# Kernel tuning notes

Hardware: AMD Instinct MI355X
Metric: run time of the kernel (lower is better)

The kernel has to match this reference:

```python
import jax, jax.numpy as jnp
import numpy as np

# head layout: lcmap(2) | lcoff(2) | lleng(1) | angle(1) -> head_off = [2,4,5,6]
NLINES = 1000       # top-K line centers per image (F-Clip default)
RESOLUTION = 128    # heatmap resolution (512 image / 4), M.resolution
S_NMS = 2.0         # structural NMS threshold, M.s_nms


def _heatmap_nms(h):
    # keep only 3x3 local maxima (standard center-point heatmap NMS)
    hmax = jax.lax.reduce_window(h, -jnp.inf, jax.lax.max, (3, 3), (1, 1), 'SAME')
    return jnp.where(h == hmax, h, 0.0)


def _fclip_single(lcmap, lcoff, lleng, angle):
    # lcmap (H,W); lcoff (2,H,W); lleng (H,W); angle (H,W)
    H, W = lcmap.shape
    score, idx = jax.lax.top_k(_heatmap_nms(lcmap).reshape(-1), NLINES)
    yi, xi = idx // W, idx % W
    # sub-pixel line center: integer cell + learned offset + 0.5
    yc = yi.astype(lcmap.dtype) + lcoff[0, yi, xi] + 0.5
    xc = xi.astype(lcmap.dtype) + lcoff[1, yi, xi] + 0.5
    half_len = lleng[yi, xi] * (RESOLUTION / 2.0)   # length normalized by res/2
    theta = angle[yi, xi] * jnp.pi                  # angle normalized [0,1] -> [0,pi]
    dy = half_len * jnp.sin(theta)
    dx = half_len * jnp.cos(theta)
    p1 = jnp.stack([yc - dy, xc - dx], axis=-1)     # (K,2) in (y,x)
    p2 = jnp.stack([yc + dy, xc + dx], axis=-1)
    lines = jnp.stack([p1, p2], axis=1)             # (K,2,2)
    return lines, score


def _structure_nms(lines, score, thr):
    # structural distance between lines = min over the two endpoint matchings
    p1, p2 = lines[:, 0], lines[:, 1]               # (K,2) each

    def sq(a, b):                                   # pairwise squared dists (K,K)
        return ((a[:, None, :] - b[None, :, :]) ** 2).sum(-1)

    dist = jnp.minimum(sq(p1, p1) + sq(p2, p2), sq(p1, p2) + sq(p2, p1))
    K = score.shape[0]
    i = jnp.arange(K)
    # scores arrive sorted descending from top_k: line j is suppressed by any
    # higher-scoring line i<j within the structural threshold
    suppress = jnp.any((dist <= thr) & (i[:, None] < i[None, :]), axis=0)
    return lines, jnp.where(suppress, 0.0, score)


def setup_inputs() -> dict:
    key = jax.random.key(0)
    # raw head logits from the backbone stack: (B, 6, H, W)
    output = jax.random.normal(key, (32, 6, 128, 128), dtype=jnp.float32)
    return {"output": output}


def reference(output):
    # GLSD.test_forward decode path
    lcmap = jax.nn.softmax(output[:, 0:2], axis=1)[:, 1]   # (B,H,W) center prob
    lcoff = jax.nn.sigmoid(output[:, 2:4]) - 0.5           # (B,2,H,W) offsets
    lleng = jax.nn.sigmoid(output[:, 4])                   # (B,H,W) half length
    angle = jax.nn.sigmoid(output[:, 5])                   # (B,H,W) angle
    lines, score = jax.vmap(_fclip_single)(lcmap, lcoff, lleng, angle)
    lines, score = jax.vmap(lambda l, s: _structure_nms(l, s, S_NMS))(lines, score)
    return lcmap, lcoff, lleng, angle, lines, score
```

## Files before the change

kernel.cpp:

```cpp
#include <hip/hip_runtime.h>
#include <math.h>

#define BATCH 32
#define HW 16384
#define WIDTH 128
#define NLINES 1000
#define NCAND 4096
#define CHUNK 1024
#define NCHUNK 4
#define SLOTS_PER_BLOCK 64

#define OFF_LCMAP 0
#define OFF_LCOFF (BATCH * HW)
#define OFF_LLENG (OFF_LCOFF + 2 * BATCH * HW)
#define OFF_ANGLE (OFF_LLENG + BATCH * HW)
#define OFF_LINES (OFF_ANGLE + BATCH * HW)
#define OFF_SCORE (OFF_LINES + BATCH * NLINES * 4)

#define WS_NEEDED ((size_t)BATCH * NCAND * 8)

#define PI_F 3.14159265358979323846f

#define NMS_KTILE 16
#define NMS_NSPLIT 16
#define NMS_SPLIT 63

__device__ __forceinline__ float sigmoidf_(float x) {
    return 1.0f / (1.0f + expf(-x));
}

__device__ __forceinline__ float softmax1(float x0, float x1) {
    float m = fmaxf(x0, x1);
    float e0 = expf(x0 - m);
    float e1 = expf(x1 - m);
    return e1 / (e0 + e1);
}

__device__ __forceinline__ unsigned long long pack_key(float v, unsigned p) {
    return ((unsigned long long)__float_as_uint(v) << 32)
         | (unsigned long long)(0xFFFFFFFFu - p);
}

__global__ __launch_bounds__(256) void prep_collect_kernel(
        const float* __restrict__ in, float* __restrict__ out,
        unsigned long long* __restrict__ wskeys) {
    __shared__ float sm[4][WIDTH];
    __shared__ int wcnt_s[4];
    __shared__ int wpre_s[4];
    __shared__ int tot_s;

    const int blk = blockIdx.x;
    const int b = blk >> 6;
    const int rp = blk & 63;
    const int y0 = rp * 2;
    const int r = threadIdx.x >> 7;
    const int c = threadIdx.x & (WIDTH - 1);
    const int y = y0 + r;
    const int p = y * WIDTH + c;
    const float* __restrict__ ib = in + (size_t)b * 6 * HW;

    float x0 = ib[p];
    float x1 = ib[HW + p];
    float x2 = ib[2 * HW + p];
    float x3 = ib[3 * HW + p];
    float x4 = ib[4 * HW + p];
    float x5 = ib[5 * HW + p];

    float v = softmax1(x0, x1);
    sm[1 + r][c] = v;
    {
        int hy = (r == 0) ? (y0 - 1) : (y0 + 2);
        int hyc = min(max(hy, 0), WIDTH - 1);
        int hp = hyc * WIDTH + c;
        sm[r == 0 ? 0 : 3][c] = softmax1(ib[hp], ib[HW + hp]);
    }

    out[OFF_LCMAP + b * HW + p] = v;
    out[OFF_LCOFF + b * 2 * HW + p]      = sigmoidf_(x2) - 0.5f;
    out[OFF_LCOFF + b * 2 * HW + HW + p] = sigmoidf_(x3) - 0.5f;
    out[OFF_LLENG + b * HW + p] = sigmoidf_(x4);
    out[OFF_ANGLE + b * HW + p] = sigmoidf_(x5);
    __syncthreads();

    const int ly = 1 + r;
    float m = -INFINITY;
    #pragma unroll
    for (int dy = -1; dy <= 1; ++dy) {
        #pragma unroll
        for (int dx = -1; dx <= 1; ++dx) {
            if (dy == 0 && dx == 0) continue;
            int yy = y + dy, xx = c + dx;
            int xc = min(max(xx, 0), WIDTH - 1);
            float nv = sm[ly + dy][xc];
            bool inb = ((unsigned)yy < (unsigned)WIDTH) & ((unsigned)xx < (unsigned)WIDTH);
            m = fmaxf(m, inb ? nv : -INFINITY);
        }
    }
    bool keep = (v >= m);

    unsigned long long mask = __ballot(keep);
    int lane = threadIdx.x & 63;
    int w = threadIdx.x >> 6;
    if (lane == 0) wcnt_s[w] = __popcll(mask);
    __syncthreads();
    if (threadIdx.x == 0) {
        int a0 = wcnt_s[0], a1 = wcnt_s[1], a2 = wcnt_s[2], a3 = wcnt_s[3];
        wpre_s[0] = 0; wpre_s[1] = a0; wpre_s[2] = a0 + a1; wpre_s[3] = a0 + a1 + a2;
        tot_s = a0 + a1 + a2 + a3;
    }
    __syncthreads();

    unsigned long long* __restrict__ gk =
        wskeys + (size_t)b * NCAND + (size_t)rp * SLOTS_PER_BLOCK;
    if (keep) {
        int pos = wpre_s[w] + __popcll(mask & ((1ULL << lane) - 1ULL));
        if (pos < SLOTS_PER_BLOCK)
            gk[pos] = pack_key(v, (unsigned)p);
    }
    int tot = tot_s < SLOTS_PER_BLOCK ? tot_s : SLOTS_PER_BLOCK;
    if (threadIdx.x < SLOTS_PER_BLOCK && threadIdx.x >= tot)
        gk[threadIdx.x] = 0ULL;
}

__global__ __launch_bounds__(512) void sort_chunks_kernel(
        unsigned long long* __restrict__ wskeys) {
    __shared__ unsigned long long sk[CHUNK];
    const int c = blockIdx.x, b = blockIdx.y;
    const int base = c * CHUNK;
    unsigned long long* gk = wskeys + (size_t)b * NCAND;

    for (int i = threadIdx.x; i < CHUNK; i += 512) sk[i] = gk[base + i];
    __syncthreads();

    for (int size = 2; size <= CHUNK; size <<= 1) {
        for (int stride = size >> 1; stride > 0; stride >>= 1) {
            int t = threadIdx.x;
            int i = ((t & ~(stride - 1)) << 1) | (t & (stride - 1));
            int j = i | stride;
            bool asc = (i & size) != 0;
            unsigned long long a = sk[i], cc = sk[j];
            if ((a < cc) != asc) { sk[i] = cc; sk[j] = a; }
            __syncthreads();
        }
    }
    for (int i = threadIdx.x; i < CHUNK; i += 512) gk[base + i] = sk[i];
}

__device__ bool keep_at(const float* __restrict__ L, int p) {
    int y = p >> 7, x = p & (WIDTH - 1);
    float v = L[p];
    for (int dy = -1; dy <= 1; ++dy) {
        int yy = y + dy;
        if (yy < 0 || yy >= WIDTH) continue;
        for (int dx = -1; dx <= 1; ++dx) {
            if (dy == 0 && dx == 0) continue;
            int xx = x + dx;
            if (xx < 0 || xx >= WIDTH) continue;
            if (L[yy * WIDTH + xx] > v) return false;
        }
    }
    return true;
}

__global__ __launch_bounds__(256) void merge_lines_kernel(
        float* __restrict__ out, const unsigned long long* __restrict__ wskeys) {
    __shared__ unsigned long long sk[NCAND];
    __shared__ int wsum[4];
    __shared__ int cnt_s;
    const int c = blockIdx.x, b = blockIdx.y;
    const unsigned long long* gk = wskeys + (size_t)b * NCAND;
    for (int i = threadIdx.x; i < NCAND; i += 256) sk[i] = gk[i];
    __syncthreads();

    const float* off0 = out + OFF_LCOFF + b * 2 * HW;
    const float* off1 = off0 + HW;
    const float* leng = out + OFF_LLENG + b * HW;
    const float* ang  = out + OFF_ANGLE + b * HW;

    #pragma unroll
    for (int q = 0; q < CHUNK / 256; ++q) {
        int lslot = q * 256 + threadIdx.x;
        int mslot = c * CHUNK + lslot;
        unsigned long long e = sk[mslot];
        if (e == 0ULL) continue;
        int rank = lslot;
        #pragma unroll
        for (int c2 = 0; c2 < NCHUNK; ++c2) {
            if (c2 == c) continue;
            const unsigned long long* A = sk + c2 * CHUNK;
            int lo = 0, hi = CHUNK;
            while (lo < hi) {
                int mid = (lo + hi) >> 1;
                if (A[mid] > e) lo = mid + 1; else hi = mid;
            }
            rank += lo;
        }
        if (rank < NLINES) {
            unsigned p = 0xFFFFFFFFu - (unsigned)(e & 0xFFFFFFFFull);
            float score = __uint_as_float((unsigned)(e >> 32));
            int yi = (int)(p >> 7), xi = (int)(p & (WIDTH - 1));
            float yc = (float)yi + off0[p] + 0.5f;
            float xc = (float)xi + off1[p] + 0.5f;
            float hl = leng[p] * 64.0f;
            float th = ang[p] * PI_F;
            float dy = hl * sinf(th);
            float dx = hl * cosf(th);
            float4 ln = make_float4(yc - dy, xc - dx, yc + dy, xc + dx);
            *(float4*)(out + OFF_LINES + (size_t)(b * NLINES + rank) * 4) = ln;
            out[OFF_SCORE + b * NLINES + rank] = score;
        }
    }

    if (c != 0) return;
    int local = 0;
    for (int i = threadIdx.x; i < NCAND; i += 256) local += (sk[i] != 0ULL);
    for (int off = 32; off; off >>= 1) local += __shfl_down(local, off);
    if ((threadIdx.x & 63) == 0) wsum[threadIdx.x >> 6] = local;
    __syncthreads();
    if (threadIdx.x == 0) cnt_s = wsum[0] + wsum[1] + wsum[2] + wsum[3];
    __syncthreads();
    const int cnt = cnt_s;
    if (cnt < NLINES && threadIdx.x == 0) {
        const float* L = out + OFF_LCMAP + b * HW;
        int rank = cnt;
        for (int p = 0; p < HW && rank < NLINES; ++p) {
            if (keep_at(L, p)) continue;
            int yi = p >> 7, xi = p & (WIDTH - 1);
            float yc = (float)yi + off0[p] + 0.5f;
            float xc = (float)xi + off1[p] + 0.5f;
            float hl = leng[p] * 64.0f;
            float th = ang[p] * PI_F;
            float dy = hl * sinf(th);
            float dx = hl * cosf(th);
            float* lo = out + OFF_LINES + (size_t)(b * NLINES + rank) * 4;
            lo[0] = yc - dy; lo[1] = xc - dx; lo[2] = yc + dy; lo[3] = xc + dx;
            out[OFF_SCORE + b * NLINES + rank] = 0.0f;
            ++rank;
        }
    }
}

__global__ __launch_bounds__(256) void nms_kernel(float* __restrict__ out) {
    __shared__ float4 lsv[NLINES];
    __shared__ unsigned char flags[NMS_KTILE][NMS_NSPLIT];
    const int tile = blockIdx.x, b = blockIdx.y;
    const float4* lg = (const float4*)(out + OFF_LINES + (size_t)b * NLINES * 4);
    for (int i = threadIdx.x; i < NLINES; i += 256) lsv[i] = lg[i];
    __syncthreads();

    const int kl = threadIdx.x & (NMS_KTILE - 1);
    const int s  = threadIdx.x >> 4;
    const int k  = tile * NMS_KTILE + kl;
    float4 P = lsv[k < NLINES ? k : 0];

    int istart = s * NMS_SPLIT;
    int iend = min(NMS_SPLIT * (s + 1), min(k, NLINES));
    bool sup = false;
    for (int i = istart; i < iend; ++i) {
        float4 Q = lsv[i];
        float a1 = __fadd_rn(__fmul_rn(Q.x - P.x, Q.x - P.x),
                             __fmul_rn(Q.y - P.y, Q.y - P.y));
        float a2 = __fadd_rn(__fmul_rn(Q.z - P.z, Q.z - P.z),
                             __fmul_rn(Q.w - P.w, Q.w - P.w));
        float d1 = __fadd_rn(a1, a2);
        float b1 = __fadd_rn(__fmul_rn(Q.x - P.z, Q.x - P.z),
                             __fmul_rn(Q.y - P.w, Q.y - P.w));
        float b2 = __fadd_rn(__fmul_rn(Q.z - P.x, Q.z - P.x),
                             __fmul_rn(Q.w - P.y, Q.w - P.y));
        float d2 = __fadd_rn(b1, b2);
        sup |= (fminf(d1, d2) <= 2.0f);
    }
    flags[kl][s] = (unsigned char)sup;
    __syncthreads();

    if (s == 0 && k < NLINES) {
        int any = 0;
        #pragma unroll
        for (int i = 0; i < NMS_NSPLIT; ++i) any |= flags[kl][i];
        float sc = out[OFF_SCORE + b * NLINES + k];
        out[OFF_SCORE + b * NLINES + k] = any ? 0.0f : sc;
    }
}

extern "C" void kernel_launch(void* const* d_in, const int* in_sizes, int n_in,
                              void* d_out, int out_size, void* d_ws, size_t ws_size,
                              hipStream_t stream) {
    const float* in = (const float*)d_in[0];
    float* out = (float*)d_out;
    (void)in_sizes; (void)n_in; (void)out_size;

    if (d_ws == nullptr || ws_size < WS_NEEDED) return;
    unsigned long long* wskeys = (unsigned long long*)d_ws;

    prep_collect_kernel<<<BATCH * 64, 256, 0, stream>>>(in, out, wskeys);
    sort_chunks_kernel<<<dim3(NCHUNK, BATCH), 512, 0, stream>>>(wskeys);
    merge_lines_kernel<<<dim3(NCHUNK, BATCH), 256, 0, stream>>>(out, wskeys);
    nms_kernel<<<dim3(64, BATCH), 256, 0, stream>>>(out);
}
```

Before: 51.00 us.

## Fuse chunk bitonic sort and merge-rank into one per-image kernel

Merges the per-chunk bitonic sort kernel and the merge/line-decode kernel into a single 1024-thread block per image. The block sorts all four chunks in shared memory and then ranks and decodes candidates directly. This removes one kernel launch and the global write and re-read of sorted keys. The cost is fewer blocks (32 instead of 128 per stage), so the GPU runs at lower parallelism, and each thread does two compare-swaps per sort step.

```diff
diff --git a/kernel.cpp b/kernel.cpp
--- a/kernel.cpp
+++ b/kernel.cpp
@@ -120,30 +120,6 @@
     int tot = tot_s < SLOTS_PER_BLOCK ? tot_s : SLOTS_PER_BLOCK;
     if (threadIdx.x < SLOTS_PER_BLOCK && threadIdx.x >= tot)
         gk[threadIdx.x] = 0ULL;
-}
-
-__global__ __launch_bounds__(512) void sort_chunks_kernel(
-        unsigned long long* __restrict__ wskeys) {
-    __shared__ unsigned long long sk[CHUNK];
-    const int c = blockIdx.x, b = blockIdx.y;
-    const int base = c * CHUNK;
-    unsigned long long* gk = wskeys + (size_t)b * NCAND;
-
-    for (int i = threadIdx.x; i < CHUNK; i += 512) sk[i] = gk[base + i];
-    __syncthreads();
-
-    for (int size = 2; size <= CHUNK; size <<= 1) {
-        for (int stride = size >> 1; stride > 0; stride >>= 1) {
-            int t = threadIdx.x;
-            int i = ((t & ~(stride - 1)) << 1) | (t & (stride - 1));
-            int j = i | stride;
-            bool asc = (i & size) != 0;
-            unsigned long long a = sk[i], cc = sk[j];
-            if ((a < cc) != asc) { sk[i] = cc; sk[j] = a; }
-            __syncthreads();
-        }
-    }
-    for (int i = threadIdx.x; i < CHUNK; i += 512) gk[base + i] = sk[i];
 }
 
 __device__ bool keep_at(const float* __restrict__ L, int p) {
@@ -162,27 +138,47 @@
     return true;
 }
 
-__global__ __launch_bounds__(256) void merge_lines_kernel(
+__global__ __launch_bounds__(1024) void sortmerge_lines_kernel(
         float* __restrict__ out, const unsigned long long* __restrict__ wskeys) {
     __shared__ unsigned long long sk[NCAND];
-    __shared__ int wsum[4];
+    __shared__ int wsum[16];
     __shared__ int cnt_s;
-    const int c = blockIdx.x, b = blockIdx.y;
+    const int b = blockIdx.x;
     const unsigned long long* gk = wskeys + (size_t)b * NCAND;
-    for (int i = threadIdx.x; i < NCAND; i += 256) sk[i] = gk[i];
-    __syncthreads();
+    for (int i = threadIdx.x; i < NCAND; i += 1024) sk[i] = gk[i];
+    __syncthreads();
+
+    for (int size = 2; size <= CHUNK; size <<= 1) {
+        for (int stride = size >> 1; stride > 0; stride >>= 1) {
+            #pragma unroll
+            for (int pp = 0; pp < 2; ++pp) {
+                int t = threadIdx.x + (pp << 10);
+                int chunk = t >> 9;
+                int u = t & 511;
+                int il = ((u & ~(stride - 1)) << 1) | (u & (stride - 1));
+                int gi = chunk * CHUNK + il;
+                int gj = gi | stride;
+                bool asc = (il & size) != 0;
+                unsigned long long a = sk[gi], cc = sk[gj];
+                if ((a < cc) != asc) { sk[gi] = cc; sk[gj] = a; }
+            }
+            __syncthreads();
+        }
+    }
 
     const float* off0 = out + OFF_LCOFF + b * 2 * HW;
     const float* off1 = off0 + HW;
     const float* leng = out + OFF_LLENG + b * HW;
     const float* ang  = out + OFF_ANGLE + b * HW;
 
+    int nz = 0;
     #pragma unroll
-    for (int q = 0; q < CHUNK / 256; ++q) {
-        int lslot = q * 256 + threadIdx.x;
+    for (int c = 0; c < NCHUNK; ++c) {
+        int lslot = threadIdx.x;
         int mslot = c * CHUNK + lslot;
         unsigned long long e = sk[mslot];
         if (e == 0ULL) continue;
+        ++nz;
         int rank = lslot;
         #pragma unroll
         for (int c2 = 0; c2 < NCHUNK; ++c2) {
@@ -211,15 +207,18 @@
         }
     }
 
-    if (c != 0) return;
-    int local = 0;
-    for (int i = threadIdx.x; i < NCAND; i += 256) local += (sk[i] != 0ULL);
-    for (int off = 32; off; off >>= 1) local += __shfl_down(local, off);
-    if ((threadIdx.x & 63) == 0) wsum[threadIdx.x >> 6] = local;
-    __syncthreads();
-    if (threadIdx.x == 0) cnt_s = wsum[0] + wsum[1] + wsum[2] + wsum[3];
+    for (int off = 32; off; off >>= 1) nz += __shfl_down(nz, off);
+    if ((threadIdx.x & 63) == 0) wsum[threadIdx.x >> 6] = nz;
+    __syncthreads();
+    if (threadIdx.x == 0) {
+        int s = 0;
+        #pragma unroll
+        for (int i = 0; i < 16; ++i) s += wsum[i];
+        cnt_s = s;
+    }
     __syncthreads();
     const int cnt = cnt_s;
+
     if (cnt < NLINES && threadIdx.x == 0) {
         const float* L = out + OFF_LCMAP + b * HW;
         int rank = cnt;
@@ -293,7 +292,6 @@
     unsigned long long* wskeys = (unsigned long long*)d_ws;
 
     prep_collect_kernel<<<BATCH * 64, 256, 0, stream>>>(in, out, wskeys);
-    sort_chunks_kernel<<<dim3(NCHUNK, BATCH), 512, 0, stream>>>(wskeys);
-    merge_lines_kernel<<<dim3(NCHUNK, BATCH), 256, 0, stream>>>(out, wskeys);
+    sortmerge_lines_kernel<<<BATCH, 1024, 0, stream>>>(out, wskeys);
     nms_kernel<<<dim3(64, BATCH), 256, 0, stream>>>(out);
 }
```

After: 65.05 us. 1.28x slower.
